# Kernel optimization log

Hardware: AMD Instinct MI355X
Metric: run time of the kernel (lower is better)

Reference implementation:

```python
import jax, jax.numpy as jnp
import numpy as np

D_MODEL = 512
D_STATE = 64
HEADDIM = 64
EXPAND = 2
D_CONV = 4
D_INNER = EXPAND * D_MODEL            # 1024
NHEADS = D_INNER // HEADDIM           # 16
CONV_DIM = D_INNER + 2 * D_STATE      # 1152 (x, B, C share the depthwise conv)
D_IN_PROJ = 2 * D_INNER + 2 * D_STATE + NHEADS  # z, xBC, dt
C_IN = 512


def setup_inputs() -> dict:
    key = jax.random.key(0)
    ks = jax.random.split(key, 10)
    hs = jax.random.normal(ks[0], (1, C_IN, 16, 16, 16), jnp.float32)
    return {
        "hidden_states": hs,
        # 1x1 conv projections (weight stored as (out,in))
        "proj_in_w": jax.random.normal(ks[1], (D_MODEL, C_IN), jnp.float32) / np.float32(np.sqrt(C_IN)),
        "proj_in_b": jnp.zeros((D_MODEL,), jnp.float32),
        "proj_out_w": jax.random.normal(ks[2], (C_IN, D_MODEL), jnp.float32) * jnp.float32(0.02),
        "proj_out_b": jnp.zeros((C_IN,), jnp.float32),
        # Mamba2 core params
        "in_proj_w": jax.random.normal(ks[3], (D_IN_PROJ, D_MODEL), jnp.float32) / np.float32(np.sqrt(D_MODEL)),
        "conv_w": jax.random.normal(ks[4], (CONV_DIM, D_CONV), jnp.float32) / np.float32(np.sqrt(D_CONV)),
        "conv_b": jnp.zeros((CONV_DIM,), jnp.float32),
        "dt_bias": jnp.log(jnp.expm1(jax.random.uniform(ks[5], (NHEADS,), jnp.float32, 1e-3, 0.1))),
        "A_log": jnp.log(jax.random.uniform(ks[6], (NHEADS,), jnp.float32, 1.0, 16.0)),
        "D": jnp.ones((NHEADS,), jnp.float32),
        "norm_w": jnp.ones((D_INNER,), jnp.float32),
        "out_proj_w": jax.random.normal(ks[7], (D_MODEL, D_INNER), jnp.float32) / np.float32(np.sqrt(D_INNER)),
    }


def _mamba2(x, in_proj_w, conv_w, conv_b, dt_bias, A_log, Dp, norm_w, out_proj_w):
    # x: (N, T, d_model) with N = B*H*W (independent pixel sequences over time)
    N, T, _ = x.shape
    zxbcdt = jnp.einsum('ntd,ed->nte', x, in_proj_w)  # (N,T,D_IN_PROJ)
    z = zxbcdt[..., :D_INNER]
    xBC = zxbcdt[..., D_INNER:D_INNER + CONV_DIM]
    dt = zxbcdt[..., D_INNER + CONV_DIM:]             # (N,T,NHEADS)
    # causal depthwise conv along T (kernel D_CONV, left-padded), then SiLU
    pad = jnp.pad(xBC, ((0, 0), (D_CONV - 1, 0), (0, 0)))
    xc = sum(pad[:, k:k + T, :] * conv_w[:, k] for k in range(D_CONV))
    xBC = jax.nn.silu(xc + conv_b)
    xs = xBC[..., :D_INNER].reshape(N, T, NHEADS, HEADDIM)
    Bm = xBC[..., D_INNER:D_INNER + D_STATE]          # (N,T,D_STATE), ngroups=1
    Cm = xBC[..., D_INNER + D_STATE:]                 # (N,T,D_STATE)
    dt = jax.nn.softplus(dt + dt_bias)                # (N,T,NHEADS)
    A = -jnp.exp(A_log)                               # (NHEADS,)

    def step(h, inp):
        # h: (N, NHEADS, HEADDIM, D_STATE)
        dt_t, x_t, B_t, C_t = inp
        dA = jnp.exp(dt_t * A)                        # (N,NHEADS)
        h = h * dA[:, :, None, None] + (dt_t[:, :, None] * x_t)[..., None] * B_t[:, None, None, :]
        y_t = jnp.einsum('nhps,ns->nhp', h, C_t)      # (N,NHEADS,HEADDIM)
        return h, y_t

    h0 = jnp.zeros((N, NHEADS, HEADDIM, D_STATE), x.dtype)
    _, ys = jax.lax.scan(step, h0, (dt.swapaxes(0, 1), xs.swapaxes(0, 1), Bm.swapaxes(0, 1), Cm.swapaxes(0, 1)))
    y = ys.swapaxes(0, 1) + Dp[None, None, :, None] * xs   # skip term
    # gated RMSNorm: norm(y * silu(z)) * weight
    y = y.reshape(N, T, D_INNER) * jax.nn.silu(z)
    y = y * jax.lax.rsqrt(jnp.mean(y * y, axis=-1, keepdims=True) + 1e-5) * norm_w
    return jnp.einsum('ntd,od->nto', y, out_proj_w)


def reference(hidden_states, proj_in_w, proj_in_b, proj_out_w, proj_out_b,
              in_proj_w, conv_w, conv_b, dt_bias, A_log, D, norm_w, out_proj_w):
    B, C, T, H, W = hidden_states.shape
    # proj_in: 1x1 conv over channels == per-pixel matmul
    x = jnp.einsum('bcthw,dc->bthwd', hidden_states, proj_in_w) + proj_in_b
    # (B,T,H,W,D) -> (B*H*W, T, D): each pixel becomes a temporal sequence
    x = x.transpose(0, 2, 3, 1, 4).reshape(B * H * W, T, D_MODEL)
    y = _mamba2(x, in_proj_w, conv_w, conv_b, dt_bias, A_log, D, norm_w, out_proj_w)
    y = y.reshape(B, H, W, T, D_MODEL).transpose(0, 3, 1, 2, 4)  # (B,T,H,W,D)
    out = jnp.einsum('bthwd,cd->bcthw', y, proj_out_w) + proj_out_b[None, :, None, None, None]
    return (out,)
```

## Files before the change

### kernel.cpp

```cpp
#include <hip/hip_runtime.h>
#include <hip/hip_bf16.h>
#include <math.h>

#define TT       16
#define NSEQ     256
#define TOK      4096
#define DMODEL   512
#define DINNER   1024
#define DSTATE   64
#define NHEADS   16
#define HEADDIM  64
#define CONVDIM  1152
#define DINPROJ  2192
#define DTOFF    2176
#define ZLD      2176

using bf16x8 = __attribute__((ext_vector_type(8))) short;
using f32x4  = __attribute__((ext_vector_type(4))) float;
typedef __hip_bfloat16 bf16;

__device__ __forceinline__ void gload_lds16(const void* g, void* l) {
    __builtin_amdgcn_global_load_lds(
        (const __attribute__((address_space(1))) unsigned int*)g,
        (__attribute__((address_space(3))) unsigned int*)l,
        16, 0, 0);
}

template<int NFRAG>
__device__ __forceinline__ void gemm_core(
    short* As, short* Bs,
    const bf16* __restrict__ A, const bf16* __restrict__ B,
    const float* __restrict__ bias, bf16* __restrict__ Ch,
    int bm, int bn, int K, int lda, int ldb, int ldc, int Nreal)
{
    constexpr int BN = NFRAG * 32;
    const int tid = threadIdx.x;
    const int wv = tid >> 6, ln = tid & 63;
    const int m0 = bm * 128, n0 = bn * BN;
    const int wr = wv >> 1, wc = wv & 1;
    const int lr = ln & 15, lk = (ln >> 4) * 8;

    f32x4 acc[4][NFRAG];
#pragma unroll
    for (int m = 0; m < 4; ++m)
#pragma unroll
        for (int n = 0; n < NFRAG; ++n) acc[m][n] = (f32x4){0.f, 0.f, 0.f, 0.f};

    for (int k0 = 0; k0 < K; k0 += 32) {
        __syncthreads();
#pragma unroll
        for (int r = 0; r < 2; ++r) {
            const int ofs = r * 4096 + tid * 16;
            const int row = ofs >> 6;
            const int ke  = (ofs & 63) >> 1;
            gload_lds16(A + (size_t)(m0 + row) * lda + k0 + ke, (char*)As + ofs);
        }
#pragma unroll
        for (int r = 0; r < NFRAG / 2; ++r) {
            const int ofs = r * 4096 + tid * 16;
            const int row = ofs >> 6;
            const int ke  = (ofs & 63) >> 1;
            gload_lds16(B + (size_t)(n0 + row) * ldb + k0 + ke, (char*)Bs + ofs);
        }
        __syncthreads();

        bf16x8 af[4], bfr[NFRAG];
#pragma unroll
        for (int m = 0; m < 4; ++m)
            af[m] = *(const bf16x8*)&As[(wr * 64 + m * 16 + lr) * 32 + lk];
#pragma unroll
        for (int n = 0; n < NFRAG; ++n)
            bfr[n] = *(const bf16x8*)&Bs[(wc * (BN / 2) + n * 16 + lr) * 32 + lk];
#pragma unroll
        for (int m = 0; m < 4; ++m)
#pragma unroll
            for (int n = 0; n < NFRAG; ++n)
                acc[m][n] = __builtin_amdgcn_mfma_f32_16x16x32_bf16(
                    af[m], bfr[n], acc[m][n], 0, 0, 0);
    }

    const int mBase = m0 + wr * 64, nBase = n0 + wc * (BN / 2);
    float cbv[NFRAG];
#pragma unroll
    for (int n = 0; n < NFRAG; ++n) {
        const int col = nBase + n * 16 + lr;
        cbv[n] = (bias != nullptr && col < Nreal) ? bias[col] : 0.f;
    }
#pragma unroll
    for (int m = 0; m < 4; ++m) {
#pragma unroll
        for (int j = 0; j < 4; ++j) {
            const int row = mBase + m * 16 + (ln >> 4) * 4 + j;
#pragma unroll
            for (int n = 0; n < NFRAG; ++n) {
                const int col = nBase + n * 16 + lr;
                if (col < Nreal)
                    Ch[(size_t)row * ldc + col] =
                        __float2bfloat16(acc[m][n][j] + cbv[n]);
            }
        }
    }
}

__global__ __launch_bounds__(256) void k67_gemm(
    const bf16* __restrict__ A, const bf16* __restrict__ B,
    const float* __restrict__ bias, const float* __restrict__ rs,
    float* __restrict__ Cf, int K, int lda, int ldb, int ldc)
{
    __shared__ short As[128 * 32];
    __shared__ short Bs[64 * 32];

    const int tid = threadIdx.x;
    const int wv = tid >> 6, ln = tid & 63;
    const int m0 = blockIdx.x * 128, n0 = blockIdx.y * 64;
    const int wr = wv >> 1, wc = wv & 1;
    const int lr = ln & 15, lk = (ln >> 4) * 8;

    f32x4 acc[4][2];
#pragma unroll
    for (int m = 0; m < 4; ++m)
#pragma unroll
        for (int n = 0; n < 2; ++n) acc[m][n] = (f32x4){0.f, 0.f, 0.f, 0.f};

    for (int k0 = 0; k0 < K; k0 += 32) {
        __syncthreads();
#pragma unroll
        for (int r = 0; r < 2; ++r) {
            const int ofs = r * 4096 + tid * 16;
            const int row = ofs >> 6;
            const int ke  = (ofs & 63) >> 1;
            gload_lds16(A + (size_t)(m0 + row) * lda + k0 + ke, (char*)As + ofs);
        }
        {
            const int ofs = tid * 16;
            const int row = ofs >> 6;
            const int ke  = (ofs & 63) >> 1;
            gload_lds16(B + (size_t)(n0 + row) * ldb + k0 + ke, (char*)Bs + ofs);
        }
        __syncthreads();

        bf16x8 af[4], bfr[2];
#pragma unroll
        for (int m = 0; m < 4; ++m)
            af[m] = *(const bf16x8*)&As[(wr * 64 + m * 16 + lr) * 32 + lk];
#pragma unroll
        for (int n = 0; n < 2; ++n)
            bfr[n] = *(const bf16x8*)&Bs[(wc * 32 + n * 16 + lr) * 32 + lk];
#pragma unroll
        for (int m = 0; m < 4; ++m)
#pragma unroll
            for (int n = 0; n < 2; ++n)
                acc[m][n] = __builtin_amdgcn_mfma_f32_16x16x32_bf16(
                    af[m], bfr[n], acc[m][n], 0, 0, 0);
    }

    const int mBase = m0 + wr * 64, nBase = n0 + wc * 32;
    float scn[2];
#pragma unroll
    for (int n = 0; n < 2; ++n) {
        const int col = nBase + n * 16 + lr;
        const float4 pv = *(const float4*)(rs + (size_t)col * 4);
        scn[n] = rsqrtf((pv.x + pv.y + pv.z + pv.w) * (1.f / 1024.f) + 1e-5f);
    }
#pragma unroll
    for (int m = 0; m < 4; ++m) {
#pragma unroll
        for (int j = 0; j < 4; ++j) {
            const int row = mBase + m * 16 + (ln >> 4) * 4 + j;
            const float rb = bias[row];
#pragma unroll
            for (int n = 0; n < 2; ++n) {
                const int col = nBase + n * 16 + lr;
                Cf[(size_t)row * ldc + col] = acc[m][n][j] * scn[n] + rb;
            }
        }
    }
}

#define SZ_PI  (512 * 512)
#define SZ_PO  (512 * 512)
#define SZ_IP2 (ZLD * 512)
#define SZ_ALL (SZ_PI + SZ_PO + SZ_IP2)
#define NB_WC  128
#define NB_WB  768
#define NB_WT  512
#define NB_HT  2048
#define NB_ALL (NB_WC + NB_WB + NB_WT + NB_HT)

__global__ __launch_bounds__(256) void prep_all(
    const float* __restrict__ pi, const float* __restrict__ po,
    const float* __restrict__ op, const float* __restrict__ ip,
    const float* __restrict__ nw, const float* __restrict__ pib,
    const float* __restrict__ hs,
    bf16* __restrict__ wpi, bf16* __restrict__ wpo, bf16* __restrict__ wip,
    bf16* __restrict__ wopT, bf16* __restrict__ hsT,
    float* __restrict__ Wc, float* __restrict__ bc)
{
    __shared__ float smem[32 * 33];
    const int b = blockIdx.x, tid = threadIdx.x;

    if (b < NB_WC) {
        const int h = b >> 3, c0 = (b & 7) * 64;
        const int w = tid >> 6, l = tid & 63;
        const float* wdt = ip + (size_t)(DTOFF + h) * DMODEL;
        float acc = 0.f;
#pragma unroll 8
        for (int i = 0; i < 128; ++i) {
            const int d = w * 128 + i;
            acc = fmaf(wdt[d], pi[(size_t)d * DMODEL + c0 + l], acc);
        }
        smem[w * 64 + l] = acc;
        __syncthreads();
        if (tid < 64)
            Wc[(size_t)h * DMODEL + c0 + tid] =
                smem[tid] + smem[64 + tid] + smem[128 + tid] + smem[192 + tid];
        if ((b & 7) == 0) {
            float p = pib[tid] * wdt[tid] + pib[tid + 256] * wdt[tid + 256];
#pragma unroll
            for (int off = 32; off >= 1; off >>= 1) p += __shfl_xor(p, off);
            if ((tid & 63) == 0) smem[300 + (tid >> 6)] = p;
            __syncthreads();
            if (tid == 0)
                bc[h] = smem[300] + smem[301] + smem[302] + smem[303];
        }
    } else if (b < NB_WC + NB_WB) {
        const int wb = b - NB_WC;
        for (int idx = wb * 256 + tid; idx < SZ_ALL; idx += NB_WB * 256) {
            if (idx < SZ_PI) {
                wpi[idx] = __float2bfloat16(pi[idx]);
            } else if (idx < SZ_PI + SZ_PO) {
                int j = idx - SZ_PI; wpo[j] = __float2bfloat16(po[j]);
            } else {
                int j = idx - SZ_PI - SZ_PO;
                wip[j] = __float2bfloat16(ip[j]);
            }
        }
    } else if (b < NB_WC + NB_WB + NB_WT) {
        const int tb = b - NB_WC - NB_WB;
        const int o0 = (tb & 15) * 32, d0 = (tb >> 4) * 32;
        const int tx = tid & 31, ty = tid >> 5;
#pragma unroll
        for (int i = 0; i < 4; ++i)
            smem[(ty + 8 * i) * 33 + tx] =
                op[(size_t)(o0 + ty + 8 * i) * DINNER + d0 + tx];
        __syncthreads();
#pragma unroll
        for (int i = 0; i < 4; ++i) {
            const int d = d0 + ty + 8 * i;
            wopT[(size_t)d * DMODEL + o0 + tx] =
                __float2bfloat16(smem[tx * 33 + ty + 8 * i] * nw[d]);
        }
    } else {
        const int tb = b - NB_WC - NB_WB - NB_WT;
        const int v0 = (tb & 127) * 32, c0 = (tb >> 7) * 32;
        const int tx = tid & 31, ty = tid >> 5;
#pragma unroll
        for (int i = 0; i < 4; ++i)
            smem[(ty + 8 * i) * 33 + tx] =
                hs[(size_t)(c0 + ty + 8 * i) * TOK + v0 + tx];
        __syncthreads();
#pragma unroll
        for (int i = 0; i < 4; ++i)
            hsT[(size_t)(v0 + ty + 8 * i) * DMODEL + c0 + tx] =
                __float2bfloat16(smem[tx * 33 + ty + 8 * i]);
    }
}

__global__ __launch_bounds__(256) void gemm_p2k1(
    const bf16* __restrict__ wpo, const bf16* __restrict__ wopT,
    const bf16* __restrict__ hsT, const bf16* __restrict__ wpi,
    const float* __restrict__ pib,
    bf16* __restrict__ Wbig, bf16* __restrict__ xv_bf)
{
    __shared__ short As[128 * 32];
    __shared__ short Bs[64 * 32];
    const int b = blockIdx.x;
    if (b < 64) {
        gemm_core<2>(As, Bs, wpo, wopT, nullptr, Wbig,
                     b & 3, b >> 2, DMODEL, DMODEL, DMODEL, DINNER, DINNER);
    } else {
        const int b2 = b - 64;
        gemm_core<2>(As, Bs, hsT, wpi, pib, xv_bf,
                     b2 & 31, b2 >> 5, DMODEL, DMODEL, DMODEL, DMODEL, DMODEL);
    }
}

__global__ __launch_bounds__(256) void k2_dt(
    const bf16* __restrict__ xv_bf, const bf16* __restrict__ wip,
    const bf16* __restrict__ hsT, const float* __restrict__ Wc,
    const float* __restrict__ bc,
    bf16* __restrict__ zb, float* __restrict__ dtf)
{
    __shared__ short As[128 * 32];
    __shared__ short Bs[128 * 32];
    const int b = blockIdx.x;
    if (b < 544) {
        gemm_core<4>(As, Bs, xv_bf, wip, nullptr, zb,
                     b & 31, b >> 5, DMODEL, DMODEL, DMODEL, ZLD, ZLD);
    } else {
        const int v = b - 544;
        const int w = threadIdx.x >> 6, l = threadIdx.x & 63;
        const bf16x8 hv = *(const bf16x8*)(hsT + (size_t)v * DMODEL + l * 8);
        float hf[8];
#pragma unroll
        for (int j = 0; j < 8; ++j) {
            const unsigned int bits = ((unsigned int)(unsigned short)hv[j]) << 16;
            hf[j] = __uint_as_float(bits);
        }
#pragma unroll
        for (int hh = 0; hh < 4; ++hh) {
            const int h = w * 4 + hh;
            const float4* wr = (const float4*)(Wc + (size_t)h * DMODEL);
            const float4 w0 = wr[l * 2], w1 = wr[l * 2 + 1];
            float dot = hf[0] * w0.x + hf[1] * w0.y + hf[2] * w0.z + hf[3] * w0.w
                      + hf[4] * w1.x + hf[5] * w1.y + hf[6] * w1.z + hf[7] * w1.w;
#pragma unroll
            for (int off = 32; off >= 1; off >>= 1) dot += __shfl_xor(dot, off);
            if (l == 0) dtf[(size_t)v * 16 + h] = dot + bc[h];
        }
    }
}

__global__ __launch_bounds__(256) void ssd_kernel(
    const bf16* __restrict__ zb, const float* __restrict__ dtf,
    const float* __restrict__ conv_w, const float* __restrict__ conv_b,
    const float* __restrict__ dt_bias, const float* __restrict__ A_log,
    const float* __restrict__ Dp,
    bf16* __restrict__ gb, float* __restrict__ part)
{
    const int n = blockIdx.x, hq = blockIdx.y;
    const int tid = threadIdx.x;
    const int w = tid >> 6, p = tid & 63;
    const int h = hq * 4 + w;
    const int ch = hq * 256 + tid;

    __shared__ float Bsh[16][68];
    __shared__ float Csh[16][68];
    __shared__ float Gsh[16][16];
    __shared__ float Msh[4][256];
    __shared__ float red4[16][4];

    float ld[16];
#pragma unroll
    for (int t = 0; t < 16; ++t)
        ld[t] = __bfloat162float(zb[(size_t)(t * 256 + n) * ZLD + 1024 + ch]);

    const float cw0 = conv_w[ch * 4 + 0], cw1 = conv_w[ch * 4 + 1],
                cw2 = conv_w[ch * 4 + 2], cw3 = conv_w[ch * 4 + 3];
    const float cb = conv_b[ch];
    float xs[16];
#pragma unroll
    for (int t = 0; t < 16; ++t) {
        float a = fmaf(ld[t], cw3, cb);
        if (t >= 1) a = fmaf(ld[t - 1], cw2, a);
        if (t >= 2) a = fmaf(ld[t - 2], cw1, a);
        if (t >= 3) a = fmaf(ld[t - 3], cw0, a);
        xs[t] = a / (1.f + __expf(-a));
    }

    if (tid < 128) {
        const int cc = 1024 + tid;
        const float dw0 = conv_w[cc * 4 + 0], dw1 = conv_w[cc * 4 + 1],
                    dw2 = conv_w[cc * 4 + 2], dw3 = conv_w[cc * 4 + 3];
        const float db = conv_b[cc];
        float q0 = 0.f, q1 = 0.f, q2 = 0.f;
#pragma unroll
        for (int t = 0; t < 16; ++t) {
            const float cur =
                __bfloat162float(zb[(size_t)(t * 256 + n) * ZLD + 2048 + tid]);
            float a = fmaf(cur, dw3, db);
            a = fmaf(q2, dw2, a);
            a = fmaf(q1, dw1, a);
            a = fmaf(q0, dw0, a);
            const float val = a / (1.f + __expf(-a));
            if (tid < 64) Bsh[t][tid] = val; else Csh[t][tid - 64] = val;
            q0 = q1; q1 = q2; q2 = cur;
        }
    }

    const float a_h = -__expf(A_log[h]);
    float dtv_l = 0.f;
    if (p < 16) {
        const float raw = dtf[(size_t)(p * 256 + n) * 16 + h] + dt_bias[h];
        dtv_l = (raw > 20.f) ? raw : log1pf(__expf(raw));
    }
    float cum_l = dtv_l;
#pragma unroll
    for (int off = 1; off < 16; off <<= 1) {
        const float tmp = __shfl_up(cum_l, off);
        if (p >= off) cum_l += tmp;
    }
    __syncthreads();

    {
        const int t = tid >> 4, s = tid & 15;
        float acc = 0.f;
#pragma unroll
        for (int k = 0; k < 64; ++k)
            acc = fmaf(Csh[t][k], Bsh[s][k], acc);
        Gsh[t][s] = acc;
    }
    __syncthreads();

    float dtv_all[16], cum_all[16];
#pragma unroll
    for (int t = 0; t < 16; ++t) {
        dtv_all[t] = __shfl(dtv_l, t);
        cum_all[t] = __shfl(cum_l, t);
    }
#pragma unroll
    for (int q = 0; q < 4; ++q) {
        const int idx = p * 4 + q;
        const int t = idx >> 4, s = idx & 15;
        float m = 0.f;
        if (s <= t)
            m = __expf(a_h * (cum_all[t] - cum_all[s])) * Gsh[t][s] * dtv_all[s];
        Msh[w][idx] = m;
    }

    float zl[16];
#pragma unroll
    for (int t = 0; t < 16; ++t)
        zl[t] = __bfloat162float(zb[(size_t)(t * 256 + n) * ZLD + ch]);

    const float Dh = Dp[h];
    float g[16];
#pragma unroll
    for (int t = 0; t < 16; ++t) {
        float y = 0.f;
#pragma unroll
        for (int s = 0; s <= t; ++s)
            y = fmaf(Msh[w][t * 16 + s], xs[s], y);
        y = fmaf(Dh, xs[t], y);
        g[t] = y * (zl[t] / (1.f + __expf(-zl[t])));
    }

#pragma unroll
    for (int t = 0; t < 16; ++t) {
        float ss = g[t] * g[t];
#pragma unroll
        for (int off = 32; off >= 1; off >>= 1) ss += __shfl_xor(ss, off);
        if (p == 0) red4[t][w] = ss;
        gb[(size_t)(t * 256 + n) * DINNER + ch] = __float2bfloat16(g[t]);
    }
    __syncthreads();
    if (tid < 16)
        part[(size_t)(tid * 256 + n) * 4 + hq] =
            red4[tid][0] + red4[tid][1] + red4[tid][2] + red4[tid][3];
}

extern "C" void kernel_launch(void* const* d_in, const int* in_sizes, int n_in,
                              void* d_out, int out_size, void* d_ws, size_t ws_size,
                              hipStream_t stream) {
    const float* hs         = (const float*)d_in[0];
    const float* proj_in_w  = (const float*)d_in[1];
    const float* proj_in_b  = (const float*)d_in[2];
    const float* proj_out_w = (const float*)d_in[3];
    const float* proj_out_b = (const float*)d_in[4];
    const float* in_proj_w  = (const float*)d_in[5];
    const float* conv_w     = (const float*)d_in[6];
    const float* conv_b     = (const float*)d_in[7];
    const float* dt_bias    = (const float*)d_in[8];
    const float* A_log      = (const float*)d_in[9];
    const float* Dp         = (const float*)d_in[10];
    const float* norm_w     = (const float*)d_in[11];
    const float* out_proj_w = (const float*)d_in[12];
    float* out = (float*)d_out;

    float* ws      = (float*)d_ws;
    float* dtf     = ws;
    float* part    = dtf + (size_t)TOK * 16;
    float* Wc      = part + (size_t)TOK * 4;
    float* bc      = Wc + 16 * DMODEL;
    bf16*  hsT     = (bf16*)(bc + 16);
    bf16*  xv_bf   = hsT + (size_t)TOK * DMODEL;
    bf16*  zb      = xv_bf + (size_t)TOK * DMODEL;
    bf16*  gb      = zb + (size_t)TOK * ZLD;
    bf16*  wpi     = gb + (size_t)TOK * DINNER;
    bf16*  wpo     = wpi + SZ_PI;
    bf16*  wip     = wpo + SZ_PO;
    bf16*  wopT    = wip + SZ_IP2;
    bf16*  Wbig    = wopT + (size_t)DINNER * DMODEL;

    prep_all<<<NB_ALL, 256, 0, stream>>>(
        proj_in_w, proj_out_w, out_proj_w, in_proj_w, norm_w, proj_in_b, hs,
        wpi, wpo, wip, wopT, hsT, Wc, bc);

    gemm_p2k1<<<320, 256, 0, stream>>>(
        wpo, wopT, hsT, wpi, proj_in_b, Wbig, xv_bf);

    k2_dt<<<544 + TOK, 256, 0, stream>>>(
        xv_bf, wip, hsT, Wc, bc, zb, dtf);

    ssd_kernel<<<dim3(NSEQ, 4), 256, 0, stream>>>(
        zb, dtf, conv_w, conv_b, dt_bias, A_log, Dp, gb, part);

    k67_gemm<<<dim3(4, 64), 256, 0, stream>>>(
        Wbig, gb, proj_out_b, part, out, DINNER, DINNER, DINNER, TOK);
}
```

Before: 100.4 us.

## Fold proj_in weights into in_proj to skip the activation projection GEMM

Precomputes a fused weight Wfuse = in_proj_w · proj_in_w (2176x512) and a fused bias zbias = in_proj_w · proj_in_b, so the z/xBC projection reads hsT directly. This removes the per-token proj_in GEMM (4096x512x512) and the xv_bf intermediate round trip. In exchange it adds a weight-only GEMM of about 2176x512x512 plus a bias matvec and a proj_in_w transpose in the prep kernel. Precision changes slightly because the fused weight is rounded to bf16 once, instead of the intermediate activations being rounded.

```diff
diff --git a/kernel.cpp b/kernel.cpp
--- a/kernel.cpp
+++ b/kernel.cpp
@@ -177,24 +177,25 @@
     }
 }
 
-#define SZ_PI  (512 * 512)
 #define SZ_PO  (512 * 512)
 #define SZ_IP2 (ZLD * 512)
-#define SZ_ALL (SZ_PI + SZ_PO + SZ_IP2)
+#define SZ_ALL (SZ_PO + SZ_IP2)
 #define NB_WC  128
+#define NB_ZB  544
 #define NB_WB  768
+#define NB_PT  256
 #define NB_WT  512
 #define NB_HT  2048
-#define NB_ALL (NB_WC + NB_WB + NB_WT + NB_HT)
+#define NB_ALL (NB_WC + NB_ZB + NB_WB + NB_PT + NB_WT + NB_HT)
 
 __global__ __launch_bounds__(256) void prep_all(
     const float* __restrict__ pi, const float* __restrict__ po,
     const float* __restrict__ op, const float* __restrict__ ip,
     const float* __restrict__ nw, const float* __restrict__ pib,
     const float* __restrict__ hs,
-    bf16* __restrict__ wpi, bf16* __restrict__ wpo, bf16* __restrict__ wip,
-    bf16* __restrict__ wopT, bf16* __restrict__ hsT,
-    float* __restrict__ Wc, float* __restrict__ bc)
+    bf16* __restrict__ wpo, bf16* __restrict__ wip,
+    bf16* __restrict__ wpiT, bf16* __restrict__ wopT, bf16* __restrict__ hsT,
+    float* __restrict__ Wc, float* __restrict__ bc, float* __restrict__ zbias)
 {
     __shared__ float smem[32 * 33];
     const int b = blockIdx.x, tid = threadIdx.x;
@@ -223,20 +224,42 @@
             if (tid == 0)
                 bc[h] = smem[300] + smem[301] + smem[302] + smem[303];
         }
-    } else if (b < NB_WC + NB_WB) {
-        const int wb = b - NB_WC;
+    } else if (b < NB_WC + NB_ZB) {
+        const int e = (b - NB_WC) * 4 + (tid >> 6);
+        const int l = tid & 63;
+        const float* row = ip + (size_t)e * DMODEL;
+        float acc = 0.f;
+#pragma unroll
+        for (int i = 0; i < 8; ++i)
+            acc = fmaf(pib[l + i * 64], row[l + i * 64], acc);
+#pragma unroll
+        for (int off = 32; off >= 1; off >>= 1) acc += __shfl_xor(acc, off);
+        if (l == 0) zbias[e] = acc;
+    } else if (b < NB_WC + NB_ZB + NB_WB) {
+        const int wb = b - NB_WC - NB_ZB;
         for (int idx = wb * 256 + tid; idx < SZ_ALL; idx += NB_WB * 256) {
-            if (idx < SZ_PI) {
-                wpi[idx] = __float2bfloat16(pi[idx]);
-            } else if (idx < SZ_PI + SZ_PO) {
-                int j = idx - SZ_PI; wpo[j] = __float2bfloat16(po[j]);
+            if (idx < SZ_PO) {
+                wpo[idx] = __float2bfloat16(po[idx]);
             } else {
-                int j = idx - SZ_PI - SZ_PO;
+                int j = idx - SZ_PO;
                 wip[j] = __float2bfloat16(ip[j]);
             }
         }
-    } else if (b < NB_WC + NB_WB + NB_WT) {
-        const int tb = b - NB_WC - NB_WB;
+    } else if (b < NB_WC + NB_ZB + NB_WB + NB_PT) {
+        const int tb = b - NB_WC - NB_ZB - NB_WB;
+        const int c0 = (tb & 15) * 32, d0 = (tb >> 4) * 32;
+        const int tx = tid & 31, ty = tid >> 5;
+#pragma unroll
+        for (int i = 0; i < 4; ++i)
+            smem[(ty + 8 * i) * 33 + tx] =
+                pi[(size_t)(d0 + ty + 8 * i) * DMODEL + c0 + tx];
+        __syncthreads();
+#pragma unroll
+        for (int i = 0; i < 4; ++i)
+            wpiT[(size_t)(c0 + ty + 8 * i) * DMODEL + d0 + tx] =
+                __float2bfloat16(smem[tx * 33 + ty + 8 * i]);
+    } else if (b < NB_WC + NB_ZB + NB_WB + NB_PT + NB_WT) {
+        const int tb = b - NB_WC - NB_ZB - NB_WB - NB_PT;
         const int o0 = (tb & 15) * 32, d0 = (tb >> 4) * 32;
         const int tx = tid & 31, ty = tid >> 5;
 #pragma unroll
@@ -251,7 +274,7 @@
                 __float2bfloat16(smem[tx * 33 + ty + 8 * i] * nw[d]);
         }
     } else {
-        const int tb = b - NB_WC - NB_WB - NB_WT;
+        const int tb = b - NB_WC - NB_ZB - NB_WB - NB_PT - NB_WT;
         const int v0 = (tb & 127) * 32, c0 = (tb >> 7) * 32;
         const int tx = tid & 31, ty = tid >> 5;
 #pragma unroll
@@ -266,11 +289,10 @@
     }
 }
 
-__global__ __launch_bounds__(256) void gemm_p2k1(
+__global__ __launch_bounds__(256) void gemm_w(
     const bf16* __restrict__ wpo, const bf16* __restrict__ wopT,
-    const bf16* __restrict__ hsT, const bf16* __restrict__ wpi,
-    const float* __restrict__ pib,
-    bf16* __restrict__ Wbig, bf16* __restrict__ xv_bf)
+    const bf16* __restrict__ wip, const bf16* __restrict__ wpiT,
+    bf16* __restrict__ Wbig, bf16* __restrict__ Wfuse)
 {
     __shared__ short As[128 * 32];
     __shared__ short Bs[64 * 32];
@@ -280,14 +302,14 @@
                      b & 3, b >> 2, DMODEL, DMODEL, DMODEL, DINNER, DINNER);
     } else {
         const int b2 = b - 64;
-        gemm_core<2>(As, Bs, hsT, wpi, pib, xv_bf,
-                     b2 & 31, b2 >> 5, DMODEL, DMODEL, DMODEL, DMODEL, DMODEL);
+        gemm_core<2>(As, Bs, wip, wpiT, nullptr, Wfuse,
+                     b2 >> 3, b2 & 7, DMODEL, DMODEL, DMODEL, DMODEL, DMODEL);
     }
 }
 
 __global__ __launch_bounds__(256) void k2_dt(
-    const bf16* __restrict__ xv_bf, const bf16* __restrict__ wip,
-    const bf16* __restrict__ hsT, const float* __restrict__ Wc,
+    const bf16* __restrict__ hsT, const bf16* __restrict__ Wfuse,
+    const float* __restrict__ zbias, const float* __restrict__ Wc,
     const float* __restrict__ bc,
     bf16* __restrict__ zb, float* __restrict__ dtf)
 {
@@ -295,7 +317,7 @@
     __shared__ short Bs[128 * 32];
     const int b = blockIdx.x;
     if (b < 544) {
-        gemm_core<4>(As, Bs, xv_bf, wip, nullptr, zb,
+        gemm_core<4>(As, Bs, hsT, Wfuse, zbias, zb,
                      b & 31, b >> 5, DMODEL, DMODEL, DMODEL, ZLD, ZLD);
     } else {
         const int v = b - 544;
@@ -472,25 +494,25 @@
     float* part    = dtf + (size_t)TOK * 16;
     float* Wc      = part + (size_t)TOK * 4;
     float* bc      = Wc + 16 * DMODEL;
-    bf16*  hsT     = (bf16*)(bc + 16);
-    bf16*  xv_bf   = hsT + (size_t)TOK * DMODEL;
-    bf16*  zb      = xv_bf + (size_t)TOK * DMODEL;
+    float* zbias   = bc + 16;
+    bf16*  hsT     = (bf16*)(zbias + ZLD);
+    bf16*  zb      = hsT + (size_t)TOK * DMODEL;
     bf16*  gb      = zb + (size_t)TOK * ZLD;
-    bf16*  wpi     = gb + (size_t)TOK * DINNER;
-    bf16*  wpo     = wpi + SZ_PI;
+    bf16*  wpo     = gb + (size_t)TOK * DINNER;
     bf16*  wip     = wpo + SZ_PO;
     bf16*  wopT    = wip + SZ_IP2;
-    bf16*  Wbig    = wopT + (size_t)DINNER * DMODEL;
+    bf16*  wpiT    = wopT + (size_t)DINNER * DMODEL;
+    bf16*  Wfuse   = wpiT + (size_t)DMODEL * DMODEL;
+    bf16*  Wbig    = Wfuse + (size_t)ZLD * DMODEL;
 
     prep_all<<<NB_ALL, 256, 0, stream>>>(
         proj_in_w, proj_out_w, out_proj_w, in_proj_w, norm_w, proj_in_b, hs,
-        wpi, wpo, wip, wopT, hsT, Wc, bc);
-
-    gemm_p2k1<<<320, 256, 0, stream>>>(
-        wpo, wopT, hsT, wpi, proj_in_b, Wbig, xv_bf);
+        wpo, wip, wpiT, wopT, hsT, Wc, bc, zbias);
+
+    gemm_w<<<200, 256, 0, stream>>>(wpo, wopT, wip, wpiT, Wbig, Wfuse);
 
     k2_dt<<<544 + TOK, 256, 0, stream>>>(
-        xv_bf, wip, hsT, Wc, bc, zb, dtf);
+        hsT, Wfuse, zbias, Wc, bc, zb, dtf);
 
     ssd_kernel<<<dim3(NSEQ, 4), 256, 0, stream>>>(
         zb, dtf, conv_w, conv_b, dt_bias, A_log, Dp, gb, part);
```

After: 99.97 us. About the same (-0.5%).
